# Optimization experiments

Measured on AMD Instinct MI355X. Metric: run time of the kernel, lower is better.

## Reference

```python
import jax, jax.numpy as jnp
import numpy as np

N = 100000   # nodes per graph
E = 1600000  # edges (avg degree 16)
B = 2        # num_graph (batch)
F_IN = 116   # num_input
EMB = 12     # embedding dim
H = 128      # hidden_size


def setup_inputs() -> dict:
    key = jax.random.key(0)
    ks = jax.random.split(key, 8)
    node = jax.random.normal(ks[0], (B, N, F_IN), dtype=jnp.float32)
    node_type = jax.random.randint(ks[1], (N,), 0, 8, dtype=jnp.int32)
    edge_index = jax.random.randint(ks[2], (2, E), 0, N, dtype=jnp.int32)
    embed = jax.random.normal(ks[3], (8, EMB), dtype=jnp.float32)
    d1 = F_IN + EMB
    W1 = jax.random.normal(ks[4], (d1, H), dtype=jnp.float32) / np.sqrt(d1)
    b1 = jnp.zeros((H,), dtype=jnp.float32)
    W2 = jax.random.normal(ks[5], (H, H), dtype=jnp.float32) / np.sqrt(H)
    b2 = jnp.zeros((H,), dtype=jnp.float32)
    return {"node": node, "node_type": node_type, "edge_index": edge_index,
            "embed": embed, "W1": W1, "b1": b1, "W2": W2, "b2": b2}


def _gcn_conv(x, src, dst, W, b):
    """PyG GCNConv: symmetric norm with self-loops, linear (no lin bias), bias after agg.
    x: [B, N, F]; src/dst: [E] int; W: [F, H]; b: [H]."""
    n = x.shape[1]
    # degree over (A + I), computed on destination nodes
    deg = jnp.zeros((n,), x.dtype).at[dst].add(1.0) + 1.0
    dis = jax.lax.rsqrt(deg)  # deg^{-1/2}
    xw = jnp.einsum('bnf,fh->bnh', x, W)          # [B, N, H]
    norm = dis[src] * dis[dst]                    # [E]
    msgs = xw[:, src, :] * norm[None, :, None]    # [B, E, H]
    agg = jax.vmap(lambda m: jax.ops.segment_sum(m, dst, num_segments=n))(msgs)
    agg = agg + xw * (dis * dis)[None, :, None]   # self-loop contribution
    return agg + b


def reference(node, node_type, edge_index, embed, W1, b1, W2, b2):
    src, dst = edge_index[0], edge_index[1]
    emb = embed[node_type]                                      # [N, EMB]
    b = node.shape[0]
    emb_b = jnp.broadcast_to(emb[None], (b,) + emb.shape)       # repeat over batch
    x = jnp.concatenate([node, emb_b], axis=2)                  # [B, N, F_IN+EMB]
    x = jax.nn.relu(_gcn_conv(x, src, dst, W1, b1))
    # F.dropout in eval mode is identity
    x = _gcn_conv(x, src, dst, W2, b2)
    return jnp.mean(x, axis=1)                                  # [B, H]
```

## Files before the change

kernel.cpp:

```cpp
#include <hip/hip_runtime.h>
#include <stdint.h>

typedef unsigned int uint32;
typedef unsigned short ushort16;
typedef __attribute__((ext_vector_type(8))) short bf16x8;
typedef __attribute__((ext_vector_type(4))) float f32x4;
typedef __attribute__((ext_vector_type(2))) float f32x2;

#define F_IN 116
#define HID  128
#define EMBD 12
#define IDX24 0x00FFFFFFu
#define BCAP 4608
#define PCAP 6400

__device__ __forceinline__ ushort16 f2bf(float f) {
    uint32 x = __float_as_uint(f);
    uint32 r = (x + 0x7fffu + ((x >> 16) & 1u)) >> 16;
    return (ushort16)r;
}

__global__ void k_init(int* __restrict__ bcurD, int* __restrict__ bcurS,
                       float* __restrict__ partial, uint32* __restrict__ xwzrow, int K) {
    int i = blockIdx.x * 256 + threadIdx.x;
    if (i < K) { bcurD[i] = i * BCAP; bcurS[i] = i * BCAP; }
    if (blockIdx.x == 0) {
        partial[threadIdx.x] = 0.f;
        if (threadIdx.x < 64) xwzrow[threadIdx.x] = 0u;
    }
}

__global__ void k_prepB(const float* __restrict__ W1, ushort16* __restrict__ W1s) {
    int tid = blockIdx.x * blockDim.x + threadIdx.x;
    if (tid >= 2048) return;
    int q = tid & 3, n = (tid >> 2) & 15, t = (tid >> 6) & 7, kc = (tid >> 9) & 3;
    int chunk = ((kc * 8 + t) * 64 + n * 4 + q);
#pragma unroll
    for (int j = 0; j < 8; ++j) {
        int k = kc * 32 + q * 8 + j;
        W1s[chunk * 8 + j] = f2bf(W1[k * HID + t * 16 + n]);
    }
}

__global__ __launch_bounds__(256) void k_bin(
    const int* __restrict__ src, const int* __restrict__ dst,
    int* __restrict__ bcurD, int* __restrict__ bcurS,
    uint32* __restrict__ ebufD, uint32* __restrict__ ebufS, int E) {
    __shared__ int lhD[512], lbD[512], lhS[512], lbS[512];
    const int tid = threadIdx.x;
    const int e0 = blockIdx.x * 8192;
    const int eend = min(e0 + 8192, E);
    for (int i = tid; i < 512; i += 256) { lhD[i] = 0; lhS[i] = 0; }
    __syncthreads();
    for (int e = e0 + tid; e < eend; e += 256) {
        atomicAdd(&lhD[dst[e] >> 8], 1);
        atomicAdd(&lhS[src[e] >> 8], 1);
    }
    __syncthreads();
    const int rot = (blockIdx.x * 277) & 511;
#pragma unroll
    for (int i = 0; i < 2; ++i) {
        int k = (rot + tid + i * 256) & 511;
        int c = lhD[k]; lbD[k] = c ? atomicAdd(&bcurD[k], c) : 0; lhD[k] = 0;
        int d = lhS[k]; lbS[k] = d ? atomicAdd(&bcurS[k], d) : 0; lhS[k] = 0;
    }
    __syncthreads();
    for (int e = e0 + tid; e < eend; e += 256) {
        int s = src[e], d = dst[e];
        int bkD = d >> 8;
        int p = lbD[bkD] + atomicAdd(&lhD[bkD], 1);
        if (p < (bkD + 1) * BCAP) ebufD[p] = ((uint32)(d & 255) << 24) | (uint32)s;
        int bkS = s >> 8;
        int p2 = lbS[bkS] + atomicAdd(&lhS[bkS], 1);
        if (p2 < (bkS + 1) * BCAP) ebufS[p2] = ((uint32)(s & 255) << 24) | (uint32)d;
    }
}

__global__ __launch_bounds__(256) void k_csr(
    const uint32* __restrict__ ebufD, const int* __restrict__ bcurD,
    int4* __restrict__ meta, float* __restrict__ dis,
    int* __restrict__ csr, int N, int ZROW) {
    __shared__ int cnt[256];
    __shared__ int cur[256];
    __shared__ int lst[256];
    __shared__ int ps[256];
    const int b = blockIdx.x, tid = threadIdx.x;
    const int r0 = b * BCAP;
    const int r1 = min(bcurD[b], r0 + BCAP);
    cnt[tid] = 0;
    __syncthreads();
    for (int p = r0 + tid; p < r1; p += 256)
        atomicAdd(&cnt[ebufD[p] >> 24], 1);
    __syncthreads();
    const int pl = (cnt[tid] + 7) & ~7;
    ps[tid] = pl;
    __syncthreads();
    for (int off = 1; off < 256; off <<= 1) {
        int t = (tid >= off) ? ps[tid - off] : 0;
        __syncthreads();
        ps[tid] += t;
        __syncthreads();
    }
    const int start = b * PCAP + ps[tid] - pl;
    lst[tid] = start;
    cur[tid] = start;
    const int n = (b << 8) + tid;
    float dl = rsqrtf(1.0f + (float)cnt[tid]);
    if (n < N) {
        dis[n] = dl;
        meta[n] = make_int4(start, pl >> 3, __float_as_int(dl), 0);
    }
    __syncthreads();
    for (int p = r0 + tid; p < r1; p += 256) {
        uint32 v = ebufD[p];
        csr[atomicAdd(&cur[v >> 24], 1)] = (int)(v & IDX24);
    }
    __syncthreads();
    {
        int end = lst[tid] + pl;
        for (int p = cur[tid]; p < end; ++p) csr[p] = ZROW;
    }
}

__global__ __launch_bounds__(256) void k_souts(
    const uint32* __restrict__ ebufS, const int* __restrict__ bcurS,
    const float* __restrict__ dis, int4* __restrict__ meta, int N) {
    __shared__ float lso[256];
    const int b = blockIdx.x, tid = threadIdx.x;
    const int r0 = b * BCAP;
    const int r1 = min(bcurS[b], r0 + BCAP);
    lso[tid] = 0.f;
    __syncthreads();
    for (int p = r0 + tid; p < r1; p += 256) {
        uint32 v = ebufS[p];
        atomicAdd(&lso[v >> 24], dis[v & IDX24]);
    }
    __syncthreads();
    int n = (b << 8) + tid;
    if (n < N) meta[n].w = __float_as_int(lso[tid]);
}

__global__ __launch_bounds__(256, 4) void k_gemm(
    const float* __restrict__ node, const ushort16* __restrict__ W1s,
    const int* __restrict__ ntype, const float* __restrict__ embed,
    const float* __restrict__ dis, uint32* __restrict__ xw8, int N, int M)
{
    __shared__ ushort16 ldsA[4 * 4 * 64 * 8];
    __shared__ float ldis[32];
    const int tid = threadIdx.x;
    const int row0 = blockIdx.x * 64;

    if (tid < 32) {
        int n = (row0 >> 1) + tid;
        ldis[tid] = (n < N) ? dis[n] : 0.f;
    }

    const int g = tid & 31;
    const int kc0 = g >> 3, q0 = (g >> 1) & 3, half = g & 1;
#pragma unroll
    for (int j = 0; j < 8; ++j) {
        int r = (tid >> 5) + j * 8;
        int m = row0 + r;
        int n = m >> 1, b = m & 1;
        float4 v = make_float4(0.f, 0.f, 0.f, 0.f);
        if (n < N) {
            if (g < 29) v = *(const float4*)(node + ((size_t)b * N + n) * F_IN + g * 4);
            else        v = *(const float4*)(embed + ntype[n] * EMBD + (g - 29) * 4);
        }
        uint32 u0 = (uint32)f2bf(v.x) | ((uint32)f2bf(v.y) << 16);
        uint32 u1 = (uint32)f2bf(v.z) | ((uint32)f2bf(v.w) << 16);
        int mt = r >> 4, mloc = r & 15;
        int chunk = (mt * 4 + kc0) * 64 + mloc * 4 + q0;
        *(uint2*)&ldsA[chunk * 8 + half * 4] = make_uint2(u0, u1);
    }
    __syncthreads();

    const int lane = tid & 63;
    const int w = tid >> 6;
    const int fragsel = (lane & 15) * 4 + (lane >> 4);

    f32x4 acc[8];
#pragma unroll
    for (int ct = 0; ct < 8; ++ct) acc[ct] = (f32x4){0.f, 0.f, 0.f, 0.f};

#pragma unroll
    for (int kc = 0; kc < 4; ++kc) {
        bf16x8 bfr = *(const bf16x8*)&ldsA[(((w * 4 + kc) * 64) + fragsel) * 8];
#pragma unroll
        for (int ct = 0; ct < 8; ++ct) {
            bf16x8 afr = *(const bf16x8*)&W1s[(((kc * 8 + ct) * 64) + fragsel) * 8];
            acc[ct] = __builtin_amdgcn_mfma_f32_16x16x32_bf16(afr, bfr, acc[ct], 0, 0, 0);
        }
    }

    const int row = lane & 15, q = lane >> 4;
    int m = row0 + w * 16 + row;
    if (m < M) {
        float dn = ldis[(w * 16 + row) >> 1];
        uint32* rowp = xw8 + (size_t)m * 32;
#pragma unroll
        for (int ct = 0; ct < 8; ++ct) {
            f32x4 a = acc[ct];
            int u = __builtin_amdgcn_cvt_pk_fp8_f32(a[0] * dn, a[1] * dn, 0, false);
            u = __builtin_amdgcn_cvt_pk_fp8_f32(a[2] * dn, a[3] * dn, u, true);
            rowp[ct * 4 + q] = (uint32)u;
        }
    }
}

__global__ __launch_bounds__(256) void k_gather(
    const uint32* __restrict__ xw8, const int* __restrict__ csr,
    const int4* __restrict__ meta, const float* __restrict__ b1,
    float* __restrict__ partial, int N)
{
    __shared__ float sm[4][256];
    const int tid  = threadIdx.x;
    const int lane = tid & 63;
    const int wid  = tid >> 6;
    const int wv = (blockIdx.x * blockDim.x + tid) >> 6;
    const int nw = (gridDim.x * blockDim.x) >> 6;
    const int c0 = (lane & 31) * 4;
    const int slot = (lane >> 5) * HID + c0;
    const float bb0 = b1[c0], bb1 = b1[c0 + 1], bb2 = b1[c0 + 2], bb3 = b1[c0 + 3];

    float p0 = 0.f, p1 = 0.f, p2 = 0.f, p3 = 0.f;

    for (int n = wv * 2; n < N; n += nw * 2) {
        const int ns = __builtin_amdgcn_readfirstlane(n);
        const int v2 = (ns + 1 < N);
        const int4 m1 = meta[ns];
        const int4 m2 = v2 ? meta[ns + 1] : make_int4(0, 0, 0, 0);
        const int st1 = m1.x, c1 = m1.y;
        const float dn1 = __int_as_float(m1.z), so1 = __int_as_float(m1.w);
        const int st2 = m2.x, c2 = m2.y;
        const float dn2 = __int_as_float(m2.z), so2 = __int_as_float(m2.w);

        uint32 sv1 = xw8[(size_t)ns * 64 + lane];
        uint32 sv2 = v2 ? xw8[((size_t)ns + 1) * 64 + lane] : 0u;
        f32x2 lo1 = __builtin_amdgcn_cvt_pk_f32_fp8(sv1, false);
        f32x2 hi1 = __builtin_amdgcn_cvt_pk_f32_fp8(sv1, true);
        f32x2 lo2 = __builtin_amdgcn_cvt_pk_f32_fp8(sv2, false);
        f32x2 hi2 = __builtin_amdgcn_cvt_pk_f32_fp8(sv2, true);
        float a10 = lo1.x, a11 = lo1.y, a12 = hi1.x, a13 = hi1.y;
        float a20 = lo2.x, a21 = lo2.y, a22 = hi2.x, a23 = hi2.y;

        const int jm = max(c1, c2);
        for (int j = 0; j < jm; ++j) {
            if (j < c1) {
                int4 ca = *(const int4*)&csr[st1 + j * 8];
                int4 cb = *(const int4*)&csr[st1 + j * 8 + 4];
                uint32 v[8];
                v[0] = xw8[(size_t)ca.x * 64 + lane];
                v[1] = xw8[(size_t)ca.y * 64 + lane];
                v[2] = xw8[(size_t)ca.z * 64 + lane];
                v[3] = xw8[(size_t)ca.w * 64 + lane];
                v[4] = xw8[(size_t)cb.x * 64 + lane];
                v[5] = xw8[(size_t)cb.y * 64 + lane];
                v[6] = xw8[(size_t)cb.z * 64 + lane];
                v[7] = xw8[(size_t)cb.w * 64 + lane];
#pragma unroll
                for (int k = 0; k < 8; ++k) {
                    f32x2 lo = __builtin_amdgcn_cvt_pk_f32_fp8(v[k], false);
                    f32x2 hi = __builtin_amdgcn_cvt_pk_f32_fp8(v[k], true);
                    a10 += lo.x; a11 += lo.y; a12 += hi.x; a13 += hi.y;
                }
            }
            if (j < c2) {
                int4 ca = *(const int4*)&csr[st2 + j * 8];
                int4 cb = *(const int4*)&csr[st2 + j * 8 + 4];
                uint32 v[8];
                v[0] = xw8[(size_t)ca.x * 64 + lane];
                v[1] = xw8[(size_t)ca.y * 64 + lane];
                v[2] = xw8[(size_t)ca.z * 64 + lane];
                v[3] = xw8[(size_t)ca.w * 64 + lane];
                v[4] = xw8[(size_t)cb.x * 64 + lane];
                v[5] = xw8[(size_t)cb.y * 64 + lane];
                v[6] = xw8[(size_t)cb.z * 64 + lane];
                v[7] = xw8[(size_t)cb.w * 64 + lane];
#pragma unroll
                for (int k = 0; k < 8; ++k) {
                    f32x2 lo = __builtin_amdgcn_cvt_pk_f32_fp8(v[k], false);
                    f32x2 hi = __builtin_amdgcn_cvt_pk_f32_fp8(v[k], true);
                    a20 += lo.x; a21 += lo.y; a22 += hi.x; a23 += hi.y;
                }
            }
        }

        float cf1 = dn1 * (dn1 + so1);
        p0 = fmaf(cf1, fmaxf(fmaf(dn1, a10, bb0), 0.f), p0);
        p1 = fmaf(cf1, fmaxf(fmaf(dn1, a11, bb1), 0.f), p1);
        p2 = fmaf(cf1, fmaxf(fmaf(dn1, a12, bb2), 0.f), p2);
        p3 = fmaf(cf1, fmaxf(fmaf(dn1, a13, bb3), 0.f), p3);
        if (v2) {
            float cf2 = dn2 * (dn2 + so2);
            p0 = fmaf(cf2, fmaxf(fmaf(dn2, a20, bb0), 0.f), p0);
            p1 = fmaf(cf2, fmaxf(fmaf(dn2, a21, bb1), 0.f), p1);
            p2 = fmaf(cf2, fmaxf(fmaf(dn2, a22, bb2), 0.f), p2);
            p3 = fmaf(cf2, fmaxf(fmaf(dn2, a23, bb3), 0.f), p3);
        }
    }

    *(float4*)&sm[wid][slot] = make_float4(p0, p1, p2, p3);
    __syncthreads();
    if (tid < 256) {
        float s = sm[0][tid] + sm[1][tid] + sm[2][tid] + sm[3][tid];
        atomicAdd(&partial[tid], s);
    }
}

__global__ void k_final(const float* __restrict__ partial, const float* __restrict__ W2,
                        const float* __restrict__ b2, float* __restrict__ out, float invN) {
    int tid = threadIdx.x;
    int b = tid >> 7, h = tid & 127;
    float acc = 0.f;
#pragma unroll 8
    for (int k = 0; k < HID; ++k)
        acc += partial[b * HID + k] * W2[k * HID + h];
    out[tid] = acc * invN + b2[h];
}

extern "C" void kernel_launch(void* const* d_in, const int* in_sizes, int n_in,
                              void* d_out, int out_size, void* d_ws, size_t ws_size,
                              hipStream_t stream) {
    const float* node  = (const float*)d_in[0];
    const int*   ntype = (const int*)d_in[1];
    const int*   eidx  = (const int*)d_in[2];
    const float* embed = (const float*)d_in[3];
    const float* W1    = (const float*)d_in[4];
    const float* b1    = (const float*)d_in[5];
    const float* W2    = (const float*)d_in[6];
    const float* b2    = (const float*)d_in[7];
    float* out = (float*)d_out;

    const int N  = in_sizes[1];
    const int E  = in_sizes[2] / 2;
    const int B  = in_sizes[0] / (N * F_IN);
    const int M  = B * N;
    const int K  = (N + 255) >> 8;

    const int* src = eidx;
    const int* dst = eidx + E;

    char* ws = (char*)d_ws;
    size_t off = 0;
    auto alloc = [&](size_t bytes) -> void* {
        void* p = ws + off;
        off += (bytes + 255) & ~(size_t)255;
        return p;
    };
    uint32*   xw8     = (uint32*)alloc((size_t)(M + 2) * 128);
    int*      csr     = (int*)alloc((size_t)K * PCAP * sizeof(int));
    uint32*   ebufD   = (uint32*)alloc((size_t)K * BCAP * sizeof(uint32));
    uint32*   ebufS   = (uint32*)alloc((size_t)K * BCAP * sizeof(uint32));
    int4*     meta    = (int4*)alloc((size_t)N * sizeof(int4));
    float*    dis     = (float*)alloc((size_t)N * sizeof(float));
    ushort16* W1s     = (ushort16*)alloc(4 * 8 * 64 * 8 * sizeof(ushort16));
    int*      bcurD   = (int*)alloc((size_t)K * sizeof(int));
    int*      bcurS   = (int*)alloc((size_t)K * sizeof(int));
    float*    partial = (float*)alloc(2 * HID * sizeof(float));

    k_init<<<(K + 255) / 256, 256, 0, stream>>>(bcurD, bcurS, partial, xw8 + (size_t)N * 64, K);
    k_prepB<<<8, 256, 0, stream>>>(W1, W1s);
    k_bin<<<(E + 8191) / 8192, 256, 0, stream>>>(src, dst, bcurD, bcurS, ebufD, ebufS, E);
    k_csr<<<K, 256, 0, stream>>>(ebufD, bcurD, meta, dis, csr, N, N);
    k_souts<<<K, 256, 0, stream>>>(ebufS, bcurS, dis, meta, N);
    k_gemm<<<(M + 63) / 64, 256, 0, stream>>>(node, W1s, ntype, embed, dis, xw8, N, M);
    k_gather<<<2048, 256, 0, stream>>>(xw8, csr, meta, b1, partial, N);
    k_final<<<1, 256, 0, stream>>>(partial, W2, b2, out, 1.0f / (float)N);
}
```

Measured before the change: 388.0 us.

## Pad CSR rows to 16 and software-pipeline index loads in gather

Each node's CSR neighbor list is now padded to multiples of 16 instead of 8, so each gather iteration issues 16 row loads per node. The next chunk's indices are prefetched while the current rows are accumulated. Branches are removed by pointing exhausted nodes at a shared 16-entry zero-row tile set up in k_init. This raises memory-level parallelism and hides index-load latency, at the cost of more padding loads of the zero row and a larger CSR buffer.

```diff
diff --git a/kernel.cpp b/kernel.cpp
--- a/kernel.cpp
+++ b/kernel.cpp
@@ -12,7 +12,7 @@
 #define EMBD 12
 #define IDX24 0x00FFFFFFu
 #define BCAP 4608
-#define PCAP 6400
+#define PCAP 8448
 
 __device__ __forceinline__ ushort16 f2bf(float f) {
     uint32 x = __float_as_uint(f);
@@ -21,12 +21,14 @@
 }
 
 __global__ void k_init(int* __restrict__ bcurD, int* __restrict__ bcurS,
-                       float* __restrict__ partial, uint32* __restrict__ xwzrow, int K) {
+                       float* __restrict__ partial, uint32* __restrict__ xwzrow,
+                       int* __restrict__ csrz, int NZ, int K) {
     int i = blockIdx.x * 256 + threadIdx.x;
     if (i < K) { bcurD[i] = i * BCAP; bcurS[i] = i * BCAP; }
     if (blockIdx.x == 0) {
         partial[threadIdx.x] = 0.f;
         if (threadIdx.x < 64) xwzrow[threadIdx.x] = 0u;
+        if (threadIdx.x < 16) csrz[threadIdx.x] = NZ;
     }
 }
 
@@ -92,7 +94,7 @@
     for (int p = r0 + tid; p < r1; p += 256)
         atomicAdd(&cnt[ebufD[p] >> 24], 1);
     __syncthreads();
-    const int pl = (cnt[tid] + 7) & ~7;
+    const int pl = (cnt[tid] + 15) & ~15;
     ps[tid] = pl;
     __syncthreads();
     for (int off = 1; off < 256; off <<= 1) {
@@ -108,7 +110,7 @@
     float dl = rsqrtf(1.0f + (float)cnt[tid]);
     if (n < N) {
         dis[n] = dl;
-        meta[n] = make_int4(start, pl >> 3, __float_as_int(dl), 0);
+        meta[n] = make_int4(start, pl >> 4, __float_as_int(dl), 0);
     }
     __syncthreads();
     for (int p = r0 + tid; p < r1; p += 256) {
@@ -211,7 +213,7 @@
 __global__ __launch_bounds__(256) void k_gather(
     const uint32* __restrict__ xw8, const int* __restrict__ csr,
     const int4* __restrict__ meta, const float* __restrict__ b1,
-    float* __restrict__ partial, int N)
+    float* __restrict__ partial, int N, int ZT)
 {
     __shared__ float sm[4][256];
     const int tid  = threadIdx.x;
@@ -227,16 +229,16 @@
 
     for (int n = wv * 2; n < N; n += nw * 2) {
         const int ns = __builtin_amdgcn_readfirstlane(n);
-        const int v2 = (ns + 1 < N);
+        const int has2 = (ns + 1 < N);
         const int4 m1 = meta[ns];
-        const int4 m2 = v2 ? meta[ns + 1] : make_int4(0, 0, 0, 0);
+        const int4 m2 = has2 ? meta[ns + 1] : make_int4(0, 0, 0, 0);
         const int st1 = m1.x, c1 = m1.y;
         const float dn1 = __int_as_float(m1.z), so1 = __int_as_float(m1.w);
         const int st2 = m2.x, c2 = m2.y;
         const float dn2 = __int_as_float(m2.z), so2 = __int_as_float(m2.w);
 
         uint32 sv1 = xw8[(size_t)ns * 64 + lane];
-        uint32 sv2 = v2 ? xw8[((size_t)ns + 1) * 64 + lane] : 0u;
+        uint32 sv2 = has2 ? xw8[((size_t)ns + 1) * 64 + lane] : 0u;
         f32x2 lo1 = __builtin_amdgcn_cvt_pk_f32_fp8(sv1, false);
         f32x2 hi1 = __builtin_amdgcn_cvt_pk_f32_fp8(sv1, true);
         f32x2 lo2 = __builtin_amdgcn_cvt_pk_f32_fp8(sv2, false);
@@ -244,45 +246,68 @@
         float a10 = lo1.x, a11 = lo1.y, a12 = hi1.x, a13 = hi1.y;
         float a20 = lo2.x, a21 = lo2.y, a22 = hi2.x, a23 = hi2.y;
 
+        int o1 = (c1 > 0) ? st1 : ZT;
+        int o2 = (c2 > 0) ? st2 : ZT;
+        int4 A0 = *(const int4*)&csr[o1];      int4 A1 = *(const int4*)&csr[o1 + 4];
+        int4 A2 = *(const int4*)&csr[o1 + 8];  int4 A3 = *(const int4*)&csr[o1 + 12];
+        int4 B0 = *(const int4*)&csr[o2];      int4 B1 = *(const int4*)&csr[o2 + 4];
+        int4 B2 = *(const int4*)&csr[o2 + 8];  int4 B3 = *(const int4*)&csr[o2 + 12];
+
         const int jm = max(c1, c2);
         for (int j = 0; j < jm; ++j) {
-            if (j < c1) {
-                int4 ca = *(const int4*)&csr[st1 + j * 8];
-                int4 cb = *(const int4*)&csr[st1 + j * 8 + 4];
-                uint32 v[8];
-                v[0] = xw8[(size_t)ca.x * 64 + lane];
-                v[1] = xw8[(size_t)ca.y * 64 + lane];
-                v[2] = xw8[(size_t)ca.z * 64 + lane];
-                v[3] = xw8[(size_t)ca.w * 64 + lane];
-                v[4] = xw8[(size_t)cb.x * 64 + lane];
-                v[5] = xw8[(size_t)cb.y * 64 + lane];
-                v[6] = xw8[(size_t)cb.z * 64 + lane];
-                v[7] = xw8[(size_t)cb.w * 64 + lane];
-#pragma unroll
-                for (int k = 0; k < 8; ++k) {
-                    f32x2 lo = __builtin_amdgcn_cvt_pk_f32_fp8(v[k], false);
-                    f32x2 hi = __builtin_amdgcn_cvt_pk_f32_fp8(v[k], true);
-                    a10 += lo.x; a11 += lo.y; a12 += hi.x; a13 += hi.y;
-                }
+            uint32 w1[16], w2[16];
+            w1[0]  = xw8[(size_t)A0.x * 64 + lane];
+            w1[1]  = xw8[(size_t)A0.y * 64 + lane];
+            w1[2]  = xw8[(size_t)A0.z * 64 + lane];
+            w1[3]  = xw8[(size_t)A0.w * 64 + lane];
+            w1[4]  = xw8[(size_t)A1.x * 64 + lane];
+            w1[5]  = xw8[(size_t)A1.y * 64 + lane];
+            w1[6]  = xw8[(size_t)A1.z * 64 + lane];
+            w1[7]  = xw8[(size_t)A1.w * 64 + lane];
+            w1[8]  = xw8[(size_t)A2.x * 64 + lane];
+            w1[9]  = xw8[(size_t)A2.y * 64 + lane];
+            w1[10] = xw8[(size_t)A2.z * 64 + lane];
+            w1[11] = xw8[(size_t)A2.w * 64 + lane];
+            w1[12] = xw8[(size_t)A3.x * 64 + lane];
+            w1[13] = xw8[(size_t)A3.y * 64 + lane];
+            w1[14] = xw8[(size_t)A3.z * 64 + lane];
+            w1[15] = xw8[(size_t)A3.w * 64 + lane];
+            w2[0]  = xw8[(size_t)B0.x * 64 + lane];
+            w2[1]  = xw8[(size_t)B0.y * 64 + lane];
+            w2[2]  = xw8[(size_t)B0.z * 64 + lane];
+            w2[3]  = xw8[(size_t)B0.w * 64 + lane];
+            w2[4]  = xw8[(size_t)B1.x * 64 + lane];
+            w2[5]  = xw8[(size_t)B1.y * 64 + lane];
+            w2[6]  = xw8[(size_t)B1.z * 64 + lane];
+            w2[7]  = xw8[(size_t)B1.w * 64 + lane];
+            w2[8]  = xw8[(size_t)B2.x * 64 + lane];
+            w2[9]  = xw8[(size_t)B2.y * 64 + lane];
+            w2[10] = xw8[(size_t)B2.z * 64 + lane];
+            w2[11] = xw8[(size_t)B2.w * 64 + lane];
+            w2[12] = xw8[(size_t)B3.x * 64 + lane];
+            w2[13] = xw8[(size_t)B3.y * 64 + lane];
+            w2[14] = xw8[(size_t)B3.z * 64 + lane];
+            w2[15] = xw8[(size_t)B3.w * 64 + lane];
+
+            const int j1 = j + 1;
+            o1 = (j1 < c1) ? st1 + j1 * 16 : ZT;
+            o2 = (j1 < c2) ? st2 + j1 * 16 : ZT;
+            A0 = *(const int4*)&csr[o1];      A1 = *(const int4*)&csr[o1 + 4];
+            A2 = *(const int4*)&csr[o1 + 8];  A3 = *(const int4*)&csr[o1 + 12];
+            B0 = *(const int4*)&csr[o2];      B1 = *(const int4*)&csr[o2 + 4];
+            B2 = *(const int4*)&csr[o2 + 8];  B3 = *(const int4*)&csr[o2 + 12];
+
+#pragma unroll
+            for (int k = 0; k < 16; ++k) {
+                f32x2 lo = __builtin_amdgcn_cvt_pk_f32_fp8(w1[k], false);
+                f32x2 hi = __builtin_amdgcn_cvt_pk_f32_fp8(w1[k], true);
+                a10 += lo.x; a11 += lo.y; a12 += hi.x; a13 += hi.y;
             }
-            if (j < c2) {
-                int4 ca = *(const int4*)&csr[st2 + j * 8];
-                int4 cb = *(const int4*)&csr[st2 + j * 8 + 4];
-                uint32 v[8];
-                v[0] = xw8[(size_t)ca.x * 64 + lane];
-                v[1] = xw8[(size_t)ca.y * 64 + lane];
-                v[2] = xw8[(size_t)ca.z * 64 + lane];
-                v[3] = xw8[(size_t)ca.w * 64 + lane];
-                v[4] = xw8[(size_t)cb.x * 64 + lane];
-                v[5] = xw8[(size_t)cb.y * 64 + lane];
-                v[6] = xw8[(size_t)cb.z * 64 + lane];
-                v[7] = xw8[(size_t)cb.w * 64 + lane];
-#pragma unroll
-                for (int k = 0; k < 8; ++k) {
-                    f32x2 lo = __builtin_amdgcn_cvt_pk_f32_fp8(v[k], false);
-                    f32x2 hi = __builtin_amdgcn_cvt_pk_f32_fp8(v[k], true);
-                    a20 += lo.x; a21 += lo.y; a22 += hi.x; a23 += hi.y;
-                }
+#pragma unroll
+            for (int k = 0; k < 16; ++k) {
+                f32x2 lo = __builtin_amdgcn_cvt_pk_f32_fp8(w2[k], false);
+                f32x2 hi = __builtin_amdgcn_cvt_pk_f32_fp8(w2[k], true);
+                a20 += lo.x; a21 += lo.y; a22 += hi.x; a23 += hi.y;
             }
         }
 
@@ -291,7 +316,7 @@
         p1 = fmaf(cf1, fmaxf(fmaf(dn1, a11, bb1), 0.f), p1);
         p2 = fmaf(cf1, fmaxf(fmaf(dn1, a12, bb2), 0.f), p2);
         p3 = fmaf(cf1, fmaxf(fmaf(dn1, a13, bb3), 0.f), p3);
-        if (v2) {
+        if (has2) {
             float cf2 = dn2 * (dn2 + so2);
             p0 = fmaf(cf2, fmaxf(fmaf(dn2, a20, bb0), 0.f), p0);
             p1 = fmaf(cf2, fmaxf(fmaf(dn2, a21, bb1), 0.f), p1);
@@ -349,7 +374,7 @@
         return p;
     };
     uint32*   xw8     = (uint32*)alloc((size_t)(M + 2) * 128);
-    int*      csr     = (int*)alloc((size_t)K * PCAP * sizeof(int));
+    int*      csr     = (int*)alloc(((size_t)K * PCAP + 16) * sizeof(int));
     uint32*   ebufD   = (uint32*)alloc((size_t)K * BCAP * sizeof(uint32));
     uint32*   ebufS   = (uint32*)alloc((size_t)K * BCAP * sizeof(uint32));
     int4*     meta    = (int4*)alloc((size_t)N * sizeof(int4));
@@ -359,12 +384,15 @@
     int*      bcurS   = (int*)alloc((size_t)K * sizeof(int));
     float*    partial = (float*)alloc(2 * HID * sizeof(float));
 
-    k_init<<<(K + 255) / 256, 256, 0, stream>>>(bcurD, bcurS, partial, xw8 + (size_t)N * 64, K);
+    const int ZT = K * PCAP;
+
+    k_init<<<(K + 255) / 256, 256, 0, stream>>>(bcurD, bcurS, partial, xw8 + (size_t)N * 64,
+                                                csr + (size_t)ZT, N, K);
     k_prepB<<<8, 256, 0, stream>>>(W1, W1s);
     k_bin<<<(E + 8191) / 8192, 256, 0, stream>>>(src, dst, bcurD, bcurS, ebufD, ebufS, E);
     k_csr<<<K, 256, 0, stream>>>(ebufD, bcurD, meta, dis, csr, N, N);
     k_souts<<<K, 256, 0, stream>>>(ebufS, bcurS, dis, meta, N);
     k_gemm<<<(M + 63) / 64, 256, 0, stream>>>(node, W1s, ntype, embed, dis, xw8, N, M);
-    k_gather<<<2048, 256, 0, stream>>>(xw8, csr, meta, b1, partial, N);
+    k_gather<<<2048, 256, 0, stream>>>(xw8, csr, meta, b1, partial, N, ZT);
     k_final<<<1, 256, 0, stream>>>(partial, W2, b2, out, 1.0f / (float)N);
 }
```

After: 374.9 us. 1.03x faster.

## Restructure gather to 16-byte neighbor loads with 4 groups per wave

Applied to the files above, without the earlier changes.

The gather kernel now handles one node per wave. The wave is split into four 16-lane groups, each loading a whole 128-byte fp8 row per neighbour as uint4. Groups are combined with cross-lane shuffles, and the next CSR index chunk is prefetched inside the loop. CSR padding grows from 8 to 16 entries per node, with larger per-bucket capacity. Binning uses smaller edge chunks so more blocks run, and the gather grid is doubled. This aims for wider, fewer memory transactions and more parallelism, at the cost of extra padding work and shuffle reductions.

```diff
diff --git a/kernel.cpp b/kernel.cpp
--- a/kernel.cpp
+++ b/kernel.cpp
@@ -12,7 +12,7 @@
 #define EMBD 12
 #define IDX24 0x00FFFFFFu
 #define BCAP 4608
-#define PCAP 6400
+#define PCAP 8448
 
 __device__ __forceinline__ ushort16 f2bf(float f) {
     uint32 x = __float_as_uint(f);
@@ -48,8 +48,8 @@
     uint32* __restrict__ ebufD, uint32* __restrict__ ebufS, int E) {
     __shared__ int lhD[512], lbD[512], lhS[512], lbS[512];
     const int tid = threadIdx.x;
-    const int e0 = blockIdx.x * 8192;
-    const int eend = min(e0 + 8192, E);
+    const int e0 = blockIdx.x * 2048;
+    const int eend = min(e0 + 2048, E);
     for (int i = tid; i < 512; i += 256) { lhD[i] = 0; lhS[i] = 0; }
     __syncthreads();
     for (int e = e0 + tid; e < eend; e += 256) {
@@ -92,7 +92,7 @@
     for (int p = r0 + tid; p < r1; p += 256)
         atomicAdd(&cnt[ebufD[p] >> 24], 1);
     __syncthreads();
-    const int pl = (cnt[tid] + 7) & ~7;
+    const int pl = (cnt[tid] + 15) & ~15;
     ps[tid] = pl;
     __syncthreads();
     for (int off = 1; off < 256; off <<= 1) {
@@ -108,7 +108,7 @@
     float dl = rsqrtf(1.0f + (float)cnt[tid]);
     if (n < N) {
         dis[n] = dl;
-        meta[n] = make_int4(start, pl >> 3, __float_as_int(dl), 0);
+        meta[n] = make_int4(start, pl >> 4, __float_as_int(dl), 0);
     }
     __syncthreads();
     for (int p = r0 + tid; p < r1; p += 256) {
@@ -208,6 +208,12 @@
     }
 }
 
+#define ACC4(u, base) { \
+    f32x2 lo_ = __builtin_amdgcn_cvt_pk_f32_fp8((u), false); \
+    f32x2 hi_ = __builtin_amdgcn_cvt_pk_f32_fp8((u), true);  \
+    acc[(base)]     += lo_.x; acc[(base) + 1] += lo_.y;      \
+    acc[(base) + 2] += hi_.x; acc[(base) + 3] += hi_.y; }
+
 __global__ __launch_bounds__(256) void k_gather(
     const uint32* __restrict__ xw8, const int* __restrict__ csr,
     const int4* __restrict__ meta, const float* __restrict__ b1,
@@ -217,94 +223,82 @@
     const int tid  = threadIdx.x;
     const int lane = tid & 63;
     const int wid  = tid >> 6;
+    const int s    = lane & 15;
+    const int g    = lane >> 4;
     const int wv = (blockIdx.x * blockDim.x + tid) >> 6;
     const int nw = (gridDim.x * blockDim.x) >> 6;
-    const int c0 = (lane & 31) * 4;
-    const int slot = (lane >> 5) * HID + c0;
-    const float bb0 = b1[c0], bb1 = b1[c0 + 1], bb2 = b1[c0 + 2], bb3 = b1[c0 + 3];
-
-    float p0 = 0.f, p1 = 0.f, p2 = 0.f, p3 = 0.f;
-
-    for (int n = wv * 2; n < N; n += nw * 2) {
+
+    float bb[16];
+#pragma unroll
+    for (int k = 0; k < 16; ++k) bb[k] = b1[((s & 7) << 4) + k];
+
+    float p[16];
+#pragma unroll
+    for (int k = 0; k < 16; ++k) p[k] = 0.f;
+
+    for (int n = wv; n < N; n += nw) {
         const int ns = __builtin_amdgcn_readfirstlane(n);
-        const int v2 = (ns + 1 < N);
-        const int4 m1 = meta[ns];
-        const int4 m2 = v2 ? meta[ns + 1] : make_int4(0, 0, 0, 0);
-        const int st1 = m1.x, c1 = m1.y;
-        const float dn1 = __int_as_float(m1.z), so1 = __int_as_float(m1.w);
-        const int st2 = m2.x, c2 = m2.y;
-        const float dn2 = __int_as_float(m2.z), so2 = __int_as_float(m2.w);
-
-        uint32 sv1 = xw8[(size_t)ns * 64 + lane];
-        uint32 sv2 = v2 ? xw8[((size_t)ns + 1) * 64 + lane] : 0u;
-        f32x2 lo1 = __builtin_amdgcn_cvt_pk_f32_fp8(sv1, false);
-        f32x2 hi1 = __builtin_amdgcn_cvt_pk_f32_fp8(sv1, true);
-        f32x2 lo2 = __builtin_amdgcn_cvt_pk_f32_fp8(sv2, false);
-        f32x2 hi2 = __builtin_amdgcn_cvt_pk_f32_fp8(sv2, true);
-        float a10 = lo1.x, a11 = lo1.y, a12 = hi1.x, a13 = hi1.y;
-        float a20 = lo2.x, a21 = lo2.y, a22 = hi2.x, a23 = hi2.y;
-
-        const int jm = max(c1, c2);
-        for (int j = 0; j < jm; ++j) {
-            if (j < c1) {
-                int4 ca = *(const int4*)&csr[st1 + j * 8];
-                int4 cb = *(const int4*)&csr[st1 + j * 8 + 4];
-                uint32 v[8];
-                v[0] = xw8[(size_t)ca.x * 64 + lane];
-                v[1] = xw8[(size_t)ca.y * 64 + lane];
-                v[2] = xw8[(size_t)ca.z * 64 + lane];
-                v[3] = xw8[(size_t)ca.w * 64 + lane];
-                v[4] = xw8[(size_t)cb.x * 64 + lane];
-                v[5] = xw8[(size_t)cb.y * 64 + lane];
-                v[6] = xw8[(size_t)cb.z * 64 + lane];
-                v[7] = xw8[(size_t)cb.w * 64 + lane];
-#pragma unroll
-                for (int k = 0; k < 8; ++k) {
-                    f32x2 lo = __builtin_amdgcn_cvt_pk_f32_fp8(v[k], false);
-                    f32x2 hi = __builtin_amdgcn_cvt_pk_f32_fp8(v[k], true);
-                    a10 += lo.x; a11 += lo.y; a12 += hi.x; a13 += hi.y;
-                }
-            }
-            if (j < c2) {
-                int4 ca = *(const int4*)&csr[st2 + j * 8];
-                int4 cb = *(const int4*)&csr[st2 + j * 8 + 4];
-                uint32 v[8];
-                v[0] = xw8[(size_t)ca.x * 64 + lane];
-                v[1] = xw8[(size_t)ca.y * 64 + lane];
-                v[2] = xw8[(size_t)ca.z * 64 + lane];
-                v[3] = xw8[(size_t)ca.w * 64 + lane];
-                v[4] = xw8[(size_t)cb.x * 64 + lane];
-                v[5] = xw8[(size_t)cb.y * 64 + lane];
-                v[6] = xw8[(size_t)cb.z * 64 + lane];
-                v[7] = xw8[(size_t)cb.w * 64 + lane];
-#pragma unroll
-                for (int k = 0; k < 8; ++k) {
-                    f32x2 lo = __builtin_amdgcn_cvt_pk_f32_fp8(v[k], false);
-                    f32x2 hi = __builtin_amdgcn_cvt_pk_f32_fp8(v[k], true);
-                    a20 += lo.x; a21 += lo.y; a22 += hi.x; a23 += hi.y;
-                }
-            }
-        }
-
-        float cf1 = dn1 * (dn1 + so1);
-        p0 = fmaf(cf1, fmaxf(fmaf(dn1, a10, bb0), 0.f), p0);
-        p1 = fmaf(cf1, fmaxf(fmaf(dn1, a11, bb1), 0.f), p1);
-        p2 = fmaf(cf1, fmaxf(fmaf(dn1, a12, bb2), 0.f), p2);
-        p3 = fmaf(cf1, fmaxf(fmaf(dn1, a13, bb3), 0.f), p3);
-        if (v2) {
-            float cf2 = dn2 * (dn2 + so2);
-            p0 = fmaf(cf2, fmaxf(fmaf(dn2, a20, bb0), 0.f), p0);
-            p1 = fmaf(cf2, fmaxf(fmaf(dn2, a21, bb1), 0.f), p1);
-            p2 = fmaf(cf2, fmaxf(fmaf(dn2, a22, bb2), 0.f), p2);
-            p3 = fmaf(cf2, fmaxf(fmaf(dn2, a23, bb3), 0.f), p3);
-        }
-    }
-
-    *(float4*)&sm[wid][slot] = make_float4(p0, p1, p2, p3);
+        const int4 mt = meta[ns];
+        const int st = mt.x, c = mt.y;
+        const float dn = __int_as_float(mt.z), so = __int_as_float(mt.w);
+
+        const int selfrow = (g == 0) ? ns : N;
+        uint4 wsf = *(const uint4*)(xw8 + (size_t)selfrow * 64 + s * 4);
+
+        int4 ci = make_int4(N, N, N, N);
+        if (c > 0) ci = *(const int4*)&csr[st + 4 * g];
+
+        float acc[16];
+        {
+            f32x2 lo_ = __builtin_amdgcn_cvt_pk_f32_fp8(wsf.x, false);
+            f32x2 hi_ = __builtin_amdgcn_cvt_pk_f32_fp8(wsf.x, true);
+            acc[0] = lo_.x; acc[1] = lo_.y; acc[2] = hi_.x; acc[3] = hi_.y;
+            lo_ = __builtin_amdgcn_cvt_pk_f32_fp8(wsf.y, false);
+            hi_ = __builtin_amdgcn_cvt_pk_f32_fp8(wsf.y, true);
+            acc[4] = lo_.x; acc[5] = lo_.y; acc[6] = hi_.x; acc[7] = hi_.y;
+            lo_ = __builtin_amdgcn_cvt_pk_f32_fp8(wsf.z, false);
+            hi_ = __builtin_amdgcn_cvt_pk_f32_fp8(wsf.z, true);
+            acc[8] = lo_.x; acc[9] = lo_.y; acc[10] = hi_.x; acc[11] = hi_.y;
+            lo_ = __builtin_amdgcn_cvt_pk_f32_fp8(wsf.w, false);
+            hi_ = __builtin_amdgcn_cvt_pk_f32_fp8(wsf.w, true);
+            acc[12] = lo_.x; acc[13] = lo_.y; acc[14] = hi_.x; acc[15] = hi_.y;
+        }
+
+        for (int j = 0; j < c; ++j) {
+            uint4 w0 = *(const uint4*)(xw8 + (size_t)ci.x * 64 + s * 4);
+            uint4 w1 = *(const uint4*)(xw8 + (size_t)ci.y * 64 + s * 4);
+            uint4 w2 = *(const uint4*)(xw8 + (size_t)ci.z * 64 + s * 4);
+            uint4 w3 = *(const uint4*)(xw8 + (size_t)ci.w * 64 + s * 4);
+
+            const int j1 = j + 1;
+            if (j1 < c) ci = *(const int4*)&csr[st + j1 * 16 + 4 * g];
+
+            ACC4(w0.x, 0)  ACC4(w0.y, 4)  ACC4(w0.z, 8)  ACC4(w0.w, 12)
+            ACC4(w1.x, 0)  ACC4(w1.y, 4)  ACC4(w1.z, 8)  ACC4(w1.w, 12)
+            ACC4(w2.x, 0)  ACC4(w2.y, 4)  ACC4(w2.z, 8)  ACC4(w2.w, 12)
+            ACC4(w3.x, 0)  ACC4(w3.y, 4)  ACC4(w3.z, 8)  ACC4(w3.w, 12)
+        }
+
+#pragma unroll
+        for (int k = 0; k < 16; ++k) {
+            acc[k] += __shfl_xor(acc[k], 16);
+            acc[k] += __shfl_xor(acc[k], 32);
+        }
+
+        const float cf = dn * (dn + so);
+#pragma unroll
+        for (int k = 0; k < 16; ++k)
+            p[k] = fmaf(cf, fmaxf(fmaf(dn, acc[k], bb[k]), 0.f), p[k]);
+    }
+
+    if (g == 0) {
+#pragma unroll
+        for (int k = 0; k < 16; ++k) sm[wid][k * 16 + s] = p[k];
+    }
     __syncthreads();
     if (tid < 256) {
-        float s = sm[0][tid] + sm[1][tid] + sm[2][tid] + sm[3][tid];
-        atomicAdd(&partial[tid], s);
+        float t4 = sm[0][tid] + sm[1][tid] + sm[2][tid] + sm[3][tid];
+        atomicAdd(&partial[((tid & 15) << 4) + (tid >> 4)], t4);
     }
 }
 
@@ -349,7 +343,7 @@
         return p;
     };
     uint32*   xw8     = (uint32*)alloc((size_t)(M + 2) * 128);
-    int*      csr     = (int*)alloc((size_t)K * PCAP * sizeof(int));
+    int*      csr     = (int*)alloc(((size_t)K * PCAP + 16) * sizeof(int));
     uint32*   ebufD   = (uint32*)alloc((size_t)K * BCAP * sizeof(uint32));
     uint32*   ebufS   = (uint32*)alloc((size_t)K * BCAP * sizeof(uint32));
     int4*     meta    = (int4*)alloc((size_t)N * sizeof(int4));
@@ -361,10 +355,10 @@
 
     k_init<<<(K + 255) / 256, 256, 0, stream>>>(bcurD, bcurS, partial, xw8 + (size_t)N * 64, K);
     k_prepB<<<8, 256, 0, stream>>>(W1, W1s);
-    k_bin<<<(E + 8191) / 8192, 256, 0, stream>>>(src, dst, bcurD, bcurS, ebufD, ebufS, E);
+    k_bin<<<(E + 2047) / 2048, 256, 0, stream>>>(src, dst, bcurD, bcurS, ebufD, ebufS, E);
     k_csr<<<K, 256, 0, stream>>>(ebufD, bcurD, meta, dis, csr, N, N);
     k_souts<<<K, 256, 0, stream>>>(ebufS, bcurS, dis, meta, N);
     k_gemm<<<(M + 63) / 64, 256, 0, stream>>>(node, W1s, ntype, embed, dis, xw8, N, M);
-    k_gather<<<2048, 256, 0, stream>>>(xw8, csr, meta, b1, partial, N);
+    k_gather<<<4096, 256, 0, stream>>>(xw8, csr, meta, b1, partial, N);
     k_final<<<1, 256, 0, stream>>>(partial, W2, b2, out, 1.0f / (float)N);
 }
```

Result: slower. 711.4 us (+83.3%).
